# Performance work log

Hardware: AMD Instinct MI355X
Metric: run time of the kernel (lower is better)

## Reference

```python
import jax, jax.numpy as jnp
import numpy as np

N_NODES = 50000
N_EDGES = 1000000
D_NODE = 64
D_EDGE = 64


def setup_inputs() -> dict:
    key = jax.random.key(0)
    ks = jax.random.split(key, 12)
    d, de = D_NODE, D_EDGE
    din = 2 * d + de
    s = lambda f_in: 1.0 / np.sqrt(f_in)
    return {
        "node_feat": jax.random.normal(ks[0], (N_NODES, d), jnp.float32),
        "edge_src": jax.random.randint(ks[1], (N_EDGES,), 0, N_NODES, jnp.int32),
        "edge_dst": jax.random.randint(ks[2], (N_EDGES,), 0, N_NODES, jnp.int32),
        "edge_feat": jax.random.normal(ks[3], (N_EDGES, de), jnp.float32),
        # msg_mlp: Linear(din,d) -> SiLU -> Linear(d,d)
        "W_m1": jax.random.uniform(ks[4], (din, d), jnp.float32, -s(din), s(din)),
        "b_m1": jax.random.uniform(ks[5], (d,), jnp.float32, -s(din), s(din)),
        "W_m2": jax.random.uniform(ks[6], (d, d), jnp.float32, -s(d), s(d)),
        "b_m2": jax.random.uniform(ks[7], (d,), jnp.float32, -s(d), s(d)),
        # update_mlp: Linear(d,d) -> SiLU -> Linear(d,d)
        "W_u1": jax.random.uniform(ks[8], (d, d), jnp.float32, -s(d), s(d)),
        "b_u1": jax.random.uniform(ks[9], (d,), jnp.float32, -s(d), s(d)),
        "W_u2": jax.random.uniform(ks[10], (d, d), jnp.float32, -s(d), s(d)),
        "b_u2": jax.random.uniform(ks[11], (d,), jnp.float32, -s(d), s(d)),
        # LayerNorm params
        "ln_gamma": jnp.ones((d,), jnp.float32),
        "ln_beta": jnp.zeros((d,), jnp.float32),
    }


def _layer_norm(x, gamma, beta, eps=1e-5):
    mu = jnp.mean(x, axis=-1, keepdims=True)
    var = jnp.var(x, axis=-1, keepdims=True)
    return (x - mu) * jax.lax.rsqrt(var + eps) * gamma + beta


def reference(node_feat, edge_src, edge_dst, edge_feat,
              W_m1, b_m1, W_m2, b_m2, W_u1, b_u1, W_u2, b_u2,
              ln_gamma, ln_beta):
    # gather endpoint features per edge: [E, 2d+de]
    msg_input = jnp.concatenate(
        [node_feat[edge_src], node_feat[edge_dst], edge_feat], axis=-1)
    h = jax.nn.silu(msg_input @ W_m1 + b_m1)
    messages = h @ W_m2 + b_m2                      # [E, d]
    aggregated = jax.ops.segment_sum(messages, edge_dst,
                                     num_segments=node_feat.shape[0])
    upd = jax.nn.silu(aggregated @ W_u1 + b_u1) @ W_u2 + b_u2
    return _layer_norm(node_feat + upd, ln_gamma, ln_beta)
```

## Files before the change

### kernel.cpp

```cpp
#include <hip/hip_runtime.h>
#include <stdint.h>

typedef __bf16 bf16;
typedef __attribute__((ext_vector_type(8))) bf16 bf16x8;
typedef __attribute__((ext_vector_type(4))) float f32x4;

#define D 64
#define EPW 32

__device__ __forceinline__ float silu_f(float x) {
    return x / (1.0f + __expf(-x));
}

__global__ void hist_kernel(const int* __restrict__ edst, int* __restrict__ cnt, int E) {
    const int stride = gridDim.x * blockDim.x;
    for (int e = blockIdx.x * blockDim.x + threadIdx.x; e < E; e += stride)
        atomicAdd(&cnt[edst[e]], 1);
}

__global__ void scan_part_kernel(const int* __restrict__ cnt, int* __restrict__ part, int N) {
    __shared__ int red[256];
    const int t = threadIdx.x, idx = blockIdx.x * 256 + t;
    red[t] = (idx < N) ? cnt[idx] : 0;
    __syncthreads();
    for (int off = 128; off; off >>= 1) {
        if (t < off) red[t] += red[t + off];
        __syncthreads();
    }
    if (t == 0) part[blockIdx.x] = red[0];
}

__global__ void scan_base_kernel(int* __restrict__ part, int nblk) {
    __shared__ int sc[256];
    const int t = threadIdx.x;
    const int v = (t < nblk) ? part[t] : 0;
    sc[t] = v;
    __syncthreads();
    for (int off = 1; off < 256; off <<= 1) {
        int u = (t >= off) ? sc[t - off] : 0;
        __syncthreads();
        sc[t] += u;
        __syncthreads();
    }
    part[t] = sc[t] - v;
}

__global__ void scan_fin_kernel(const int* __restrict__ cnt, const int* __restrict__ part,
                                int* __restrict__ cur, int N) {
    __shared__ int sc[256];
    const int t = threadIdx.x, idx = blockIdx.x * 256 + t;
    const int v = (idx < N) ? cnt[idx] : 0;
    sc[t] = v;
    __syncthreads();
    for (int off = 1; off < 256; off <<= 1) {
        int u = (t >= off) ? sc[t - off] : 0;
        __syncthreads();
        sc[t] += u;
        __syncthreads();
    }
    if (idx < N) cur[idx] = sc[t] - v + part[blockIdx.x];
}

__global__ void scatter_kernel(const int* __restrict__ edst, int* __restrict__ cur,
                               int* __restrict__ spos, int E) {
    const int stride = gridDim.x * blockDim.x;
    for (int e = blockIdx.x * blockDim.x + threadIdx.x; e < E; e += stride) {
        int pos = atomicAdd(&cur[edst[e]], 1);
        spos[e] = pos;
    }
}

__global__ void cvt_nf_kernel(const float* __restrict__ nf, bf16* __restrict__ nfb, int total8) {
    const int i = blockIdx.x * blockDim.x + threadIdx.x;
    if (i < total8) {
        f32x4 a = ((const f32x4*)nf)[i*2], b = ((const f32x4*)nf)[i*2 + 1];
        bf16x8 v;
        #pragma unroll
        for (int k = 0; k < 4; ++k) { v[k] = (bf16)a[k]; v[4+k] = (bf16)b[k]; }
        ((bf16x8*)nfb)[i] = v;
    }
}

__global__ void permute_kernel(const int* __restrict__ esrc,
                               const int* __restrict__ edst,
                               const float* __restrict__ efeat,
                               const int* __restrict__ spos,
                               int2* __restrict__ sd,
                               bf16* __restrict__ efb,
                               int E)
{
    const int gw   = (blockIdx.x * blockDim.x + threadIdx.x) >> 6;
    const int nw   = (gridDim.x * blockDim.x) >> 6;
    const int lane = threadIdx.x & 63;
    const int sub  = lane >> 3, ch = lane & 7;

    for (int base = gw * 8; base < E; base += nw * 8) {
        const int e = base + sub;
        const bool v = e < E;
        const int ee = v ? e : E - 1;
        const int sp = spos[ee];
        const float* p = efeat + (size_t)ee * D + ch * 8;
        f32x4 x = ((const f32x4*)p)[0], y = ((const f32x4*)p)[1];
        bf16x8 o;
        #pragma unroll
        for (int i = 0; i < 4; ++i) { o[i] = (bf16)x[i]; o[4+i] = (bf16)y[i]; }
        if (v) {
            *(bf16x8*)&efb[(size_t)sp * D + ch * 8] = o;
            if (ch == 0) sd[sp] = make_int2(esrc[ee], edst[ee]);
        }
    }
}

__launch_bounds__(256, 3)
__global__ void mp_edge_sorted_kernel(
    const bf16* __restrict__ nfb,
    const int2* __restrict__ sd,
    const bf16* __restrict__ efb,
    const float* __restrict__ W1, const float* __restrict__ b1,
    const float* __restrict__ W2, const float* __restrict__ b2,
    float* __restrict__ agg,
    int E)
{
    __shared__ __align__(16) bf16 W1f[6*4*64*8];
    __shared__ __align__(16) bf16 W2f[2*4*64*8];
    __shared__ __align__(16) bf16 HM[4][32*72];
    __shared__ float b1s[D], b2s[D];

    const int t    = threadIdx.x;
    const int lane = t & 63;
    const int w    = t >> 6;
    const int g    = lane >> 4;
    const int c    = lane & 15;

    for (int idx = t; idx < 6*4*64; idx += 256) {
        int l = idx & 63, nt = (idx >> 6) & 3, ks = idx >> 8;
        int k0 = ks*32 + (l >> 4)*8, col = nt*16 + (l & 15);
        bf16x8 v;
        #pragma unroll
        for (int i = 0; i < 8; ++i) v[i] = (bf16)W1[(k0 + i)*D + col];
        *(bf16x8*)&W1f[idx*8] = v;
    }
    for (int idx = t; idx < 2*4*64; idx += 256) {
        int l = idx & 63, nt = (idx >> 6) & 3, ks = idx >> 8;
        int k0 = ks*32 + (l >> 4)*8, col = nt*16 + (l & 15);
        bf16x8 v;
        #pragma unroll
        for (int i = 0; i < 8; ++i) v[i] = (bf16)W2[(k0 + i)*D + col];
        *(bf16x8*)&W2f[idx*8] = v;
    }
    if (t < D) { b1s[t] = b1[t]; b2s[t] = b2[t]; }
    __syncthreads();

    bf16* hm = &HM[w][0];
    const int nwt = (E + EPW - 1) / EPW;

    for (int tile = blockIdx.x*4 + w; tile < nwt; tile += gridDim.x*4) {
        const int e0 = tile * EPW;
        const int r0 = min(e0 + c,      E - 1);
        const int r1 = min(e0 + 16 + c, E - 1);
        const int2 p0 = sd[r0];
        const int2 p1 = sd[r1];
        const int se0 = p0.x, de0 = p0.y;
        const int se1 = p1.x, de1 = p1.y;

        bf16x8 an[8], ae[4];
        #pragma unroll
        for (int ks = 0; ks < 4; ++ks) {
            const int row0 = (ks < 2) ? se0 : de0;
            const int row1 = (ks < 2) ? se1 : de1;
            const int coff = (ks & 1)*32 + g*8;
            an[ks*2]   = *(const bf16x8*)&nfb[(size_t)row0*D + coff];
            an[ks*2+1] = *(const bf16x8*)&nfb[(size_t)row1*D + coff];
        }
        #pragma unroll
        for (int ks2 = 0; ks2 < 2; ++ks2) {
            const int coff = ks2*32 + g*8;
            ae[ks2*2]   = *(const bf16x8*)&efb[(size_t)r0*D + coff];
            ae[ks2*2+1] = *(const bf16x8*)&efb[(size_t)r1*D + coff];
        }

        f32x4 acc0[4] = {f32x4{0,0,0,0}, f32x4{0,0,0,0}, f32x4{0,0,0,0}, f32x4{0,0,0,0}};
        f32x4 acc1[4] = {f32x4{0,0,0,0}, f32x4{0,0,0,0}, f32x4{0,0,0,0}, f32x4{0,0,0,0}};
        #pragma unroll
        for (int ks = 0; ks < 4; ++ks) {
            #pragma unroll
            for (int n = 0; n < 4; ++n) {
                bf16x8 bb = *(const bf16x8*)&W1f[((ks*4 + n)*64 + lane)*8];
                acc0[n] = __builtin_amdgcn_mfma_f32_16x16x32_bf16(an[ks*2],   bb, acc0[n], 0, 0, 0);
                acc1[n] = __builtin_amdgcn_mfma_f32_16x16x32_bf16(an[ks*2+1], bb, acc1[n], 0, 0, 0);
            }
        }
        #pragma unroll
        for (int ks2 = 0; ks2 < 2; ++ks2) {
            #pragma unroll
            for (int n = 0; n < 4; ++n) {
                bf16x8 bb = *(const bf16x8*)&W1f[(((ks2+4)*4 + n)*64 + lane)*8];
                acc0[n] = __builtin_amdgcn_mfma_f32_16x16x32_bf16(ae[ks2*2],   bb, acc0[n], 0, 0, 0);
                acc1[n] = __builtin_amdgcn_mfma_f32_16x16x32_bf16(ae[ks2*2+1], bb, acc1[n], 0, 0, 0);
            }
        }

        #pragma unroll
        for (int n = 0; n < 4; ++n) {
            const int col = n*16 + c;
            const float bias = b1s[col];
            #pragma unroll
            for (int j = 0; j < 4; ++j) {
                hm[(g*4 + j)*72 + col]      = (bf16)silu_f(acc0[n][j] + bias);
                hm[(16 + g*4 + j)*72 + col] = (bf16)silu_f(acc1[n][j] + bias);
            }
        }

        f32x4 acc2a[4] = {f32x4{0,0,0,0}, f32x4{0,0,0,0}, f32x4{0,0,0,0}, f32x4{0,0,0,0}};
        f32x4 acc2b[4] = {f32x4{0,0,0,0}, f32x4{0,0,0,0}, f32x4{0,0,0,0}, f32x4{0,0,0,0}};
        #pragma unroll
        for (int ks = 0; ks < 2; ++ks) {
            bf16x8 a0 = *(const bf16x8*)&hm[c*72        + ks*32 + g*8];
            bf16x8 a1 = *(const bf16x8*)&hm[(16 + c)*72 + ks*32 + g*8];
            #pragma unroll
            for (int n = 0; n < 4; ++n) {
                bf16x8 bb = *(const bf16x8*)&W2f[((ks*4 + n)*64 + lane)*8];
                acc2a[n] = __builtin_amdgcn_mfma_f32_16x16x32_bf16(a0, bb, acc2a[n], 0, 0, 0);
                acc2b[n] = __builtin_amdgcn_mfma_f32_16x16x32_bf16(a1, bb, acc2b[n], 0, 0, 0);
            }
        }

        asm volatile("s_waitcnt lgkmcnt(0)" ::: "memory");

        #pragma unroll
        for (int n = 0; n < 4; ++n) {
            const int col = n*16 + c;
            const float bias = b2s[col];
            #pragma unroll
            for (int j = 0; j < 4; ++j) {
                hm[(g*4 + j)*72 + col]      = (bf16)(acc2a[n][j] + bias);
                hm[(16 + g*4 + j)*72 + col] = (bf16)(acc2b[n][j] + bias);
            }
        }

        const int da = __shfl(de0, lane & 15);
        const int db = __shfl(de1, lane & 15);
        const int row = lane & 31;
        int rowd = (lane & 16) ? db : da;
        if (e0 + row >= E) rowd = -1;
        const int prevd = __shfl(rowd, (lane + 63) & 63);
        const bool st = (row == 0) || (rowd != prevd);
        unsigned long long m = __ballot(st) & 0xFFFFFFFFull;

        while (m) {
            const int a = __builtin_ctzll(m); m &= m - 1;
            const int rb = m ? __builtin_ctzll(m) : 32;
            const int d = __shfl(rowd, a);
            if (d >= 0) {
                float s = 0.f;
                for (int r = a; r < rb; ++r) s += (float)hm[r*72 + lane];
                float* dp = &agg[(size_t)d*D + lane];
                if (a > 0 && rb < 32) *dp = s;
                else atomicAdd(dp, s);
            }
        }
    }
}

__launch_bounds__(256, 3)
__global__ void mp_edge_atomic_kernel(
    const float* __restrict__ node_feat,
    const int*   __restrict__ esrc,
    const int*   __restrict__ edst,
    const float* __restrict__ efeat,
    const float* __restrict__ W1, const float* __restrict__ b1,
    const float* __restrict__ W2, const float* __restrict__ b2,
    float* __restrict__ agg,
    int E)
{
    __shared__ __align__(16) bf16 W1f[6*4*64*8];
    __shared__ __align__(16) bf16 W2f[2*4*64*8];
    __shared__ __align__(16) bf16 HM[4][32*72];
    __shared__ float b1s[D], b2s[D];

    const int t    = threadIdx.x;
    const int lane = t & 63;
    const int w    = t >> 6;
    const int g    = lane >> 4;
    const int c    = lane & 15;

    for (int idx = t; idx < 6*4*64; idx += 256) {
        int l = idx & 63, nt = (idx >> 6) & 3, ks = idx >> 8;
        int k0 = ks*32 + (l >> 4)*8, col = nt*16 + (l & 15);
        bf16x8 v;
        #pragma unroll
        for (int i = 0; i < 8; ++i) v[i] = (bf16)W1[(k0 + i)*D + col];
        *(bf16x8*)&W1f[idx*8] = v;
    }
    for (int idx = t; idx < 2*4*64; idx += 256) {
        int l = idx & 63, nt = (idx >> 6) & 3, ks = idx >> 8;
        int k0 = ks*32 + (l >> 4)*8, col = nt*16 + (l & 15);
        bf16x8 v;
        #pragma unroll
        for (int i = 0; i < 8; ++i) v[i] = (bf16)W2[(k0 + i)*D + col];
        *(bf16x8*)&W2f[idx*8] = v;
    }
    if (t < D) { b1s[t] = b1[t]; b2s[t] = b2[t]; }
    __syncthreads();

    bf16* hm = &HM[w][0];
    const int nwt = (E + EPW - 1) / EPW;

    for (int tile = blockIdx.x*4 + w; tile < nwt; tile += gridDim.x*4) {
        const int e0 = tile * EPW;
        const int r0 = min(e0 + c,      E - 1);
        const int r1 = min(e0 + 16 + c, E - 1);
        const int se0 = esrc[r0], de0 = edst[r0];
        const int se1 = esrc[r1], de1 = edst[r1];

        f32x4 acc0[4] = {f32x4{0,0,0,0}, f32x4{0,0,0,0}, f32x4{0,0,0,0}, f32x4{0,0,0,0}};
        f32x4 acc1[4] = {f32x4{0,0,0,0}, f32x4{0,0,0,0}, f32x4{0,0,0,0}, f32x4{0,0,0,0}};
        #pragma unroll
        for (int ks = 0; ks < 6; ++ks) {
            const int col = ks*32 + g*8;
            const float *p0, *p1;
            if (col < 64)       { p0 = node_feat + (size_t)se0*D + col;        p1 = node_feat + (size_t)se1*D + col; }
            else if (col < 128) { p0 = node_feat + (size_t)de0*D + (col - 64); p1 = node_feat + (size_t)de1*D + (col - 64); }
            else                { p0 = efeat + (size_t)r0*D + (col - 128);     p1 = efeat + (size_t)r1*D + (col - 128); }
            f32x4 xa = ((const f32x4*)p0)[0], xb = ((const f32x4*)p0)[1];
            f32x4 ya = ((const f32x4*)p1)[0], yb = ((const f32x4*)p1)[1];
            bf16x8 a0, a1;
            #pragma unroll
            for (int i = 0; i < 4; ++i) {
                a0[i] = (bf16)xa[i];  a0[4+i] = (bf16)xb[i];
                a1[i] = (bf16)ya[i];  a1[4+i] = (bf16)yb[i];
            }
            #pragma unroll
            for (int n = 0; n < 4; ++n) {
                bf16x8 bb = *(const bf16x8*)&W1f[((ks*4 + n)*64 + lane)*8];
                acc0[n] = __builtin_amdgcn_mfma_f32_16x16x32_bf16(a0, bb, acc0[n], 0, 0, 0);
                acc1[n] = __builtin_amdgcn_mfma_f32_16x16x32_bf16(a1, bb, acc1[n], 0, 0, 0);
            }
        }

        #pragma unroll
        for (int n = 0; n < 4; ++n) {
            const int col = n*16 + c;
            const float bias = b1s[col];
            #pragma unroll
            for (int j = 0; j < 4; ++j) {
                hm[(g*4 + j)*72 + col]      = (bf16)silu_f(acc0[n][j] + bias);
                hm[(16 + g*4 + j)*72 + col] = (bf16)silu_f(acc1[n][j] + bias);
            }
        }

        f32x4 acc2a[4] = {f32x4{0,0,0,0}, f32x4{0,0,0,0}, f32x4{0,0,0,0}, f32x4{0,0,0,0}};
        f32x4 acc2b[4] = {f32x4{0,0,0,0}, f32x4{0,0,0,0}, f32x4{0,0,0,0}, f32x4{0,0,0,0}};
        #pragma unroll
        for (int ks = 0; ks < 2; ++ks) {
            bf16x8 a0 = *(const bf16x8*)&hm[c*72        + ks*32 + g*8];
            bf16x8 a1 = *(const bf16x8*)&hm[(16 + c)*72 + ks*32 + g*8];
            #pragma unroll
            for (int n = 0; n < 4; ++n) {
                bf16x8 bb = *(const bf16x8*)&W2f[((ks*4 + n)*64 + lane)*8];
                acc2a[n] = __builtin_amdgcn_mfma_f32_16x16x32_bf16(a0, bb, acc2a[n], 0, 0, 0);
                acc2b[n] = __builtin_amdgcn_mfma_f32_16x16x32_bf16(a1, bb, acc2b[n], 0, 0, 0);
            }
        }

        #pragma unroll
        for (int j = 0; j < 4; ++j) {
            const int row = g*4 + j;
            const int d0 = __shfl(de0, row);
            const int d1 = __shfl(de1, row);
            const bool ok0 = (e0 + row)      < E;
            const bool ok1 = (e0 + 16 + row) < E;
            #pragma unroll
            for (int n = 0; n < 4; ++n) {
                const int col = n*16 + c;
                if (ok0) atomicAdd(&agg[(size_t)d0*D + col], acc2a[n][j] + b2s[col]);
                if (ok1) atomicAdd(&agg[(size_t)d1*D + col], acc2b[n][j] + b2s[col]);
            }
        }
    }
}

__launch_bounds__(256, 4)
__global__ void node_gemm_kernel(
    const float* __restrict__ node_feat,
    const float* __restrict__ Wu1, const float* __restrict__ bu1,
    const float* __restrict__ Wu2, const float* __restrict__ bu2,
    const float* __restrict__ gamma, const float* __restrict__ beta,
    float* __restrict__ inout, int N)
{
    __shared__ __align__(16) bf16 Wf1[2*4*64*8];
    __shared__ __align__(16) bf16 Wf2[2*4*64*8];
    __shared__ __align__(16) bf16 Hs[4][16*72];
    __shared__ float b1s[D], b2s[D], gs[D], bs[D];

    const int t    = threadIdx.x;
    const int lane = t & 63;
    const int w    = t >> 6;
    const int g    = lane >> 4;
    const int c    = lane & 15;

    for (int idx = t; idx < 2*4*64; idx += 256) {
        int l = idx & 63, nt = (idx >> 6) & 3, ks = idx >> 8;
        int k0 = ks*32 + (l >> 4)*8, col = nt*16 + (l & 15);
        bf16x8 v1, v2;
        #pragma unroll
        for (int i = 0; i < 8; ++i) {
            v1[i] = (bf16)Wu1[(k0 + i)*D + col];
            v2[i] = (bf16)Wu2[(k0 + i)*D + col];
        }
        *(bf16x8*)&Wf1[idx*8] = v1;
        *(bf16x8*)&Wf2[idx*8] = v2;
    }
    if (t < D) { b1s[t] = bu1[t]; b2s[t] = bu2[t]; gs[t] = gamma[t]; bs[t] = beta[t]; }
    __syncthreads();

    const int base = blockIdx.x*64 + w*16;
    if (base >= N) return;
    bf16* hs = &Hs[w][0];

    f32x4 acc[4] = {f32x4{0,0,0,0}, f32x4{0,0,0,0}, f32x4{0,0,0,0}, f32x4{0,0,0,0}};
    #pragma unroll
    for (int ks = 0; ks < 2; ++ks) {
        const int rowA = min(base + c, N - 1);
        const float* p = inout + (size_t)rowA*D + ks*32 + g*8;
        f32x4 xa = ((const f32x4*)p)[0], xb = ((const f32x4*)p)[1];
        bf16x8 a;
        #pragma unroll
        for (int i = 0; i < 4; ++i) { a[i] = (bf16)xa[i]; a[4+i] = (bf16)xb[i]; }
        #pragma unroll
        for (int n = 0; n < 4; ++n) {
            bf16x8 bb = *(const bf16x8*)&Wf1[((ks*4 + n)*64 + lane)*8];
            acc[n] = __builtin_amdgcn_mfma_f32_16x16x32_bf16(a, bb, acc[n], 0, 0, 0);
        }
    }
    #pragma unroll
    for (int n = 0; n < 4; ++n) {
        const int col = n*16 + c;
        const float bias = b1s[col];
        #pragma unroll
        for (int j = 0; j < 4; ++j)
            hs[(g*4 + j)*72 + col] = (bf16)silu_f(acc[n][j] + bias);
    }

    f32x4 acc2[4] = {f32x4{0,0,0,0}, f32x4{0,0,0,0}, f32x4{0,0,0,0}, f32x4{0,0,0,0}};
    #pragma unroll
    for (int ks = 0; ks < 2; ++ks) {
        bf16x8 a = *(const bf16x8*)&hs[c*72 + ks*32 + g*8];
        #pragma unroll
        for (int n = 0; n < 4; ++n) {
            bf16x8 bb = *(const bf16x8*)&Wf2[((ks*4 + n)*64 + lane)*8];
            acc2[n] = __builtin_amdgcn_mfma_f32_16x16x32_bf16(a, bb, acc2[n], 0, 0, 0);
        }
    }

    float y[4][4];
    #pragma unroll
    for (int n = 0; n < 4; ++n) {
        const int col = n*16 + c;
        #pragma unroll
        for (int j = 0; j < 4; ++j) {
            const int row = base + g*4 + j;
            const float x0 = (row < N) ? node_feat[(size_t)row*D + col] : 0.f;
            y[n][j] = x0 + acc2[n][j] + b2s[col];
        }
    }
    #pragma unroll
    for (int j = 0; j < 4; ++j) {
        float s1 = 0.f, s2 = 0.f;
        #pragma unroll
        for (int n = 0; n < 4; ++n) { s1 += y[n][j]; s2 += y[n][j]*y[n][j]; }
        #pragma unroll
        for (int mm = 1; mm < 16; mm <<= 1) {
            s1 += __shfl_xor(s1, mm);
            s2 += __shfl_xor(s2, mm);
        }
        const float mu  = s1 * (1.0f/64.0f);
        const float var = s2 * (1.0f/64.0f) - mu*mu;
        const float rs  = rsqrtf(var + 1e-5f);
        const int row = base + g*4 + j;
        if (row < N) {
            #pragma unroll
            for (int n = 0; n < 4; ++n) {
                const int col = n*16 + c;
                inout[(size_t)row*D + col] = (y[n][j] - mu)*rs*gs[col] + bs[col];
            }
        }
    }
}

extern "C" void kernel_launch(void* const* d_in, const int* in_sizes, int n_in,
                              void* d_out, int out_size, void* d_ws, size_t ws_size,
                              hipStream_t stream) {
    const float* node_feat = (const float*)d_in[0];
    const int*   esrc      = (const int*)d_in[1];
    const int*   edst      = (const int*)d_in[2];
    const float* efeat     = (const float*)d_in[3];
    const float* W_m1      = (const float*)d_in[4];
    const float* b_m1      = (const float*)d_in[5];
    const float* W_m2      = (const float*)d_in[6];
    const float* b_m2      = (const float*)d_in[7];
    const float* W_u1      = (const float*)d_in[8];
    const float* b_u1      = (const float*)d_in[9];
    const float* W_u2      = (const float*)d_in[10];
    const float* b_u2      = (const float*)d_in[11];
    const float* ln_gamma  = (const float*)d_in[12];
    const float* ln_beta   = (const float*)d_in[13];

    float* out = (float*)d_out;
    const int E = in_sizes[1];
    const int N = in_sizes[0] / D;

    const size_t efb_bytes = (((size_t)E * D * 2) + 255) & ~(size_t)255;
    const size_t sd_bytes  = (((size_t)E * 8) + 255) & ~(size_t)255;
    const size_t int_bytes = ((sizeof(int) * ((size_t)E + 2*(size_t)N + 256)) + 255) & ~(size_t)255;
    const size_t nfb_bytes = (((size_t)N * D * 2) + 255) & ~(size_t)255;
    const size_t need = efb_bytes + sd_bytes + int_bytes + nfb_bytes;

    const int nwt   = (E + EPW - 1) / EPW;
    const int nblk  = (nwt + 3) / 4;
    const int grid1 = nblk < 768 ? nblk : 768;
    const int gridN = (N + 63) / 64;
    const int nchunk = (N + 255) / 256;

    if (ws_size >= need) {
        bf16* efb  = (bf16*)d_ws;
        int2* sd   = (int2*)((char*)d_ws + efb_bytes);
        int*  spos = (int*)((char*)d_ws + efb_bytes + sd_bytes);
        int*  cnt  = spos + E;
        int*  cur  = cnt + N;
        int*  part = cur + N;
        bf16* nfb  = (bf16*)((char*)d_ws + efb_bytes + sd_bytes + int_bytes);

        const int total8 = N * D / 8;
        cvt_nf_kernel<<<(total8 + 255)/256, 256, 0, stream>>>(node_feat, nfb, total8);

        hipMemsetAsync(cnt, 0, sizeof(int)*(size_t)N, stream);
        hist_kernel     <<<1024, 256, 0, stream>>>(edst, cnt, E);
        scan_part_kernel<<<nchunk, 256, 0, stream>>>(cnt, part, N);
        scan_base_kernel<<<1, 256, 0, stream>>>(part, nchunk);
        scan_fin_kernel <<<nchunk, 256, 0, stream>>>(cnt, part, cur, N);
        scatter_kernel  <<<1024, 256, 0, stream>>>(edst, cur, spos, E);

        permute_kernel<<<2048, 256, 0, stream>>>(esrc, edst, efeat, spos, sd, efb, E);

        hipMemsetAsync(out, 0, (size_t)N * D * sizeof(float), stream);
        mp_edge_sorted_kernel<<<grid1, 256, 0, stream>>>(nfb, sd, efb,
                                                         W_m1, b_m1, W_m2, b_m2,
                                                         out, E);
    } else {
        hipMemsetAsync(out, 0, (size_t)N * D * sizeof(float), stream);
        mp_edge_atomic_kernel<<<grid1, 256, 0, stream>>>(node_feat, esrc, edst, efeat,
                                                         W_m1, b_m1, W_m2, b_m2,
                                                         out, E);
    }

    node_gemm_kernel<<<gridN, 256, 0, stream>>>(node_feat, W_u1, b_u1, W_u2, b_u2,
                                                ln_gamma, ln_beta, out, N);
}
```

Before: 290.7 us.

## Drop edge-feature permute pass; gather fp32 edge features by index in edge kernel

Removes the permute kernel that wrote a dst-sorted bf16 copy of edge features. The scatter kernel now writes (src, dst, original edge id) records directly, and the edge MLP kernel gathers fp32 edge features by original id and converts them to bf16 in registers. The cnt and output memsets are folded into the cvt and scan_fin kernels, removing two memset launches. The cost is random, uncoalesced fp32 edge-feature reads at twice the bytes, plus 16-byte index records, in the main kernel.

```diff
diff --git a/kernel.cpp b/kernel.cpp
--- a/kernel.cpp
+++ b/kernel.cpp
@@ -10,6 +10,20 @@
 
 __device__ __forceinline__ float silu_f(float x) {
     return x / (1.0f + __expf(-x));
+}
+
+__global__ void cvt_nf_kernel(const float* __restrict__ nf, bf16* __restrict__ nfb,
+                              int* __restrict__ cnt, int total8, int N) {
+    const int i = blockIdx.x * blockDim.x + threadIdx.x;
+    if (i < total8) {
+        f32x4 a = ((const f32x4*)nf)[i*2], b = ((const f32x4*)nf)[i*2 + 1];
+        bf16x8 v;
+        #pragma unroll
+        for (int k = 0; k < 4; ++k) { v[k] = (bf16)a[k]; v[4+k] = (bf16)b[k]; }
+        ((bf16x8*)nfb)[i] = v;
+    }
+    for (int j = blockIdx.x * blockDim.x + threadIdx.x; j < N; j += gridDim.x * blockDim.x)
+        cnt[j] = 0;
 }
 
 __global__ void hist_kernel(const int* __restrict__ edst, int* __restrict__ cnt, int E) {
@@ -46,7 +60,7 @@
 }
 
 __global__ void scan_fin_kernel(const int* __restrict__ cnt, const int* __restrict__ part,
-                                int* __restrict__ cur, int N) {
+                                int* __restrict__ cur, float* __restrict__ outz, int N) {
     __shared__ int sc[256];
     const int t = threadIdx.x, idx = blockIdx.x * 256 + t;
     const int v = (idx < N) ? cnt[idx] : 0;
@@ -58,64 +72,30 @@
         sc[t] += u;
         __syncthreads();
     }
-    if (idx < N) cur[idx] = sc[t] - v + part[blockIdx.x];
-}
-
-__global__ void scatter_kernel(const int* __restrict__ edst, int* __restrict__ cur,
-                               int* __restrict__ spos, int E) {
+    if (idx < N) {
+        cur[idx] = sc[t] - v + part[blockIdx.x];
+        f32x4 z = {0.f, 0.f, 0.f, 0.f};
+        float* o = outz + (size_t)idx * D;
+        #pragma unroll
+        for (int i = 0; i < 16; ++i) ((f32x4*)o)[i] = z;
+    }
+}
+
+__global__ void scatter_kernel(const int* __restrict__ esrc, const int* __restrict__ edst,
+                               int* __restrict__ cur, int4* __restrict__ sde, int E) {
     const int stride = gridDim.x * blockDim.x;
     for (int e = blockIdx.x * blockDim.x + threadIdx.x; e < E; e += stride) {
-        int pos = atomicAdd(&cur[edst[e]], 1);
-        spos[e] = pos;
-    }
-}
-
-__global__ void cvt_nf_kernel(const float* __restrict__ nf, bf16* __restrict__ nfb, int total8) {
-    const int i = blockIdx.x * blockDim.x + threadIdx.x;
-    if (i < total8) {
-        f32x4 a = ((const f32x4*)nf)[i*2], b = ((const f32x4*)nf)[i*2 + 1];
-        bf16x8 v;
-        #pragma unroll
-        for (int k = 0; k < 4; ++k) { v[k] = (bf16)a[k]; v[4+k] = (bf16)b[k]; }
-        ((bf16x8*)nfb)[i] = v;
-    }
-}
-
-__global__ void permute_kernel(const int* __restrict__ esrc,
-                               const int* __restrict__ edst,
-                               const float* __restrict__ efeat,
-                               const int* __restrict__ spos,
-                               int2* __restrict__ sd,
-                               bf16* __restrict__ efb,
-                               int E)
-{
-    const int gw   = (blockIdx.x * blockDim.x + threadIdx.x) >> 6;
-    const int nw   = (gridDim.x * blockDim.x) >> 6;
-    const int lane = threadIdx.x & 63;
-    const int sub  = lane >> 3, ch = lane & 7;
-
-    for (int base = gw * 8; base < E; base += nw * 8) {
-        const int e = base + sub;
-        const bool v = e < E;
-        const int ee = v ? e : E - 1;
-        const int sp = spos[ee];
-        const float* p = efeat + (size_t)ee * D + ch * 8;
-        f32x4 x = ((const f32x4*)p)[0], y = ((const f32x4*)p)[1];
-        bf16x8 o;
-        #pragma unroll
-        for (int i = 0; i < 4; ++i) { o[i] = (bf16)x[i]; o[4+i] = (bf16)y[i]; }
-        if (v) {
-            *(bf16x8*)&efb[(size_t)sp * D + ch * 8] = o;
-            if (ch == 0) sd[sp] = make_int2(esrc[ee], edst[ee]);
-        }
+        const int d = edst[e];
+        const int pos = atomicAdd(&cur[d], 1);
+        sde[pos] = make_int4(esrc[e], d, e, 0);
     }
 }
 
 __launch_bounds__(256, 3)
 __global__ void mp_edge_sorted_kernel(
     const bf16* __restrict__ nfb,
-    const int2* __restrict__ sd,
-    const bf16* __restrict__ efb,
+    const int4* __restrict__ sde,
+    const float* __restrict__ efeat,
     const float* __restrict__ W1, const float* __restrict__ b1,
     const float* __restrict__ W2, const float* __restrict__ b2,
     float* __restrict__ agg,
@@ -158,12 +138,13 @@
         const int e0 = tile * EPW;
         const int r0 = min(e0 + c,      E - 1);
         const int r1 = min(e0 + 16 + c, E - 1);
-        const int2 p0 = sd[r0];
-        const int2 p1 = sd[r1];
-        const int se0 = p0.x, de0 = p0.y;
-        const int se1 = p1.x, de1 = p1.y;
-
-        bf16x8 an[8], ae[4];
+        const int4 q0 = sde[r0];
+        const int4 q1 = sde[r1];
+        const int se0 = q0.x, de0 = q0.y, ee0 = q0.z;
+        const int se1 = q1.x, de1 = q1.y, ee1 = q1.z;
+
+        bf16x8 an[8];
+        f32x4  ef[8];
         #pragma unroll
         for (int ks = 0; ks < 4; ++ks) {
             const int row0 = (ks < 2) ? se0 : de0;
@@ -175,8 +156,12 @@
         #pragma unroll
         for (int ks2 = 0; ks2 < 2; ++ks2) {
             const int coff = ks2*32 + g*8;
-            ae[ks2*2]   = *(const bf16x8*)&efb[(size_t)r0*D + coff];
-            ae[ks2*2+1] = *(const bf16x8*)&efb[(size_t)r1*D + coff];
+            const float* p0 = efeat + (size_t)ee0*D + coff;
+            const float* p1 = efeat + (size_t)ee1*D + coff;
+            ef[ks2*4+0] = ((const f32x4*)p0)[0];
+            ef[ks2*4+1] = ((const f32x4*)p0)[1];
+            ef[ks2*4+2] = ((const f32x4*)p1)[0];
+            ef[ks2*4+3] = ((const f32x4*)p1)[1];
         }
 
         f32x4 acc0[4] = {f32x4{0,0,0,0}, f32x4{0,0,0,0}, f32x4{0,0,0,0}, f32x4{0,0,0,0}};
@@ -192,11 +177,19 @@
         }
         #pragma unroll
         for (int ks2 = 0; ks2 < 2; ++ks2) {
+            bf16x8 a0, a1;
+            #pragma unroll
+            for (int i = 0; i < 4; ++i) {
+                a0[i]   = (bf16)ef[ks2*4+0][i];
+                a0[4+i] = (bf16)ef[ks2*4+1][i];
+                a1[i]   = (bf16)ef[ks2*4+2][i];
+                a1[4+i] = (bf16)ef[ks2*4+3][i];
+            }
             #pragma unroll
             for (int n = 0; n < 4; ++n) {
                 bf16x8 bb = *(const bf16x8*)&W1f[(((ks2+4)*4 + n)*64 + lane)*8];
-                acc0[n] = __builtin_amdgcn_mfma_f32_16x16x32_bf16(ae[ks2*2],   bb, acc0[n], 0, 0, 0);
-                acc1[n] = __builtin_amdgcn_mfma_f32_16x16x32_bf16(ae[ks2*2+1], bb, acc1[n], 0, 0, 0);
+                acc0[n] = __builtin_amdgcn_mfma_f32_16x16x32_bf16(a0, bb, acc0[n], 0, 0, 0);
+                acc1[n] = __builtin_amdgcn_mfma_f32_16x16x32_bf16(a1, bb, acc1[n], 0, 0, 0);
             }
         }
 
@@ -510,11 +503,10 @@
     const int E = in_sizes[1];
     const int N = in_sizes[0] / D;
 
-    const size_t efb_bytes = (((size_t)E * D * 2) + 255) & ~(size_t)255;
-    const size_t sd_bytes  = (((size_t)E * 8) + 255) & ~(size_t)255;
-    const size_t int_bytes = ((sizeof(int) * ((size_t)E + 2*(size_t)N + 256)) + 255) & ~(size_t)255;
+    const size_t sde_bytes = (((size_t)E * 16) + 255) & ~(size_t)255;
+    const size_t int_bytes = ((sizeof(int) * (2*(size_t)N + 256)) + 255) & ~(size_t)255;
     const size_t nfb_bytes = (((size_t)N * D * 2) + 255) & ~(size_t)255;
-    const size_t need = efb_bytes + sd_bytes + int_bytes + nfb_bytes;
+    const size_t need = sde_bytes + int_bytes + nfb_bytes;
 
     const int nwt   = (E + EPW - 1) / EPW;
     const int nblk  = (nwt + 3) / 4;
@@ -523,28 +515,21 @@
     const int nchunk = (N + 255) / 256;
 
     if (ws_size >= need) {
-        bf16* efb  = (bf16*)d_ws;
-        int2* sd   = (int2*)((char*)d_ws + efb_bytes);
-        int*  spos = (int*)((char*)d_ws + efb_bytes + sd_bytes);
-        int*  cnt  = spos + E;
+        int4* sde  = (int4*)d_ws;
+        int*  cnt  = (int*)((char*)d_ws + sde_bytes);
         int*  cur  = cnt + N;
         int*  part = cur + N;
-        bf16* nfb  = (bf16*)((char*)d_ws + efb_bytes + sd_bytes + int_bytes);
+        bf16* nfb  = (bf16*)((char*)d_ws + sde_bytes + int_bytes);
 
         const int total8 = N * D / 8;
-        cvt_nf_kernel<<<(total8 + 255)/256, 256, 0, stream>>>(node_feat, nfb, total8);
-
-        hipMemsetAsync(cnt, 0, sizeof(int)*(size_t)N, stream);
+        cvt_nf_kernel   <<<(total8 + 255)/256, 256, 0, stream>>>(node_feat, nfb, cnt, total8, N);
         hist_kernel     <<<1024, 256, 0, stream>>>(edst, cnt, E);
         scan_part_kernel<<<nchunk, 256, 0, stream>>>(cnt, part, N);
         scan_base_kernel<<<1, 256, 0, stream>>>(part, nchunk);
-        scan_fin_kernel <<<nchunk, 256, 0, stream>>>(cnt, part, cur, N);
-        scatter_kernel  <<<1024, 256, 0, stream>>>(edst, cur, spos, E);
-
-        permute_kernel<<<2048, 256, 0, stream>>>(esrc, edst, efeat, spos, sd, efb, E);
-
-        hipMemsetAsync(out, 0, (size_t)N * D * sizeof(float), stream);
-        mp_edge_sorted_kernel<<<grid1, 256, 0, stream>>>(nfb, sd, efb,
+        scan_fin_kernel <<<nchunk, 256, 0, stream>>>(cnt, part, cur, out, N);
+        scatter_kernel  <<<1024, 256, 0, stream>>>(esrc, edst, cur, sde, E);
+
+        mp_edge_sorted_kernel<<<grid1, 256, 0, stream>>>(nfb, sde, efeat,
                                                          W_m1, b_m1, W_m2, b_m2,
                                                          out, E);
     } else {
```

New measurement: 262.2 us. 9.8% less time.
